# Optimization experiments

Hardware: AMD Instinct MI355X
Metric: run time of the kernel (lower is better)

## Reference

```python
import jax, jax.numpy as jnp
import numpy as np

NS, NW, E, DIN, OUT, H = 100_000, 400_000, 500_000, 64, 64, 4


def setup_inputs() -> dict:
    key = jax.random.key(0)
    ks = jax.random.split(key, 26)
    s = 1.0 / np.sqrt(DIN)
    sg = 1.0 / np.sqrt(OUT)
    inp = {
        "x_sites": jax.random.normal(ks[0], (NS, DIN), jnp.float32),
        "x_wells": jax.random.normal(ks[1], (NW, DIN), jnp.float32),
        "edge_sw_src": jax.random.randint(ks[2], (E,), 0, NS, jnp.int32),
        "edge_sw_dst": jax.random.randint(ks[3], (E,), 0, NW, jnp.int32),
        "edge_ws_src": jax.random.randint(ks[4], (E,), 0, NW, jnp.int32),
        "edge_ws_dst": jax.random.randint(ks[5], (E,), 0, NS, jnp.int32),
        # GAT ('pfas_sites','distance','gw_wells'), heads=4, concat=False
        "W_sw": jax.random.normal(ks[6], (DIN, H * OUT), jnp.float32) * s,
        "att_src_sw": jax.random.normal(ks[7], (H, OUT), jnp.float32) * sg,
        "att_dst_sw": jax.random.normal(ks[8], (H, OUT), jnp.float32) * sg,
        "b_sw": jnp.zeros((OUT,), jnp.float32),
        # SAGE ('gw_wells','distance','pfas_sites')
        "Wl_ws": jax.random.normal(ks[9], (DIN, OUT), jnp.float32) * s,
        "bl_ws": jnp.zeros((OUT,), jnp.float32),
        "Wr_ws": jax.random.normal(ks[10], (DIN, OUT), jnp.float32) * s,
        # GAT ('pfas_sites','self_loop','pfas_sites'), add_self_loops=True -> identity edges
        "W_ss": jax.random.normal(ks[11], (DIN, H * OUT), jnp.float32) * s,
        "att_src_ss": jax.random.normal(ks[12], (H, OUT), jnp.float32) * sg,
        "att_dst_ss": jax.random.normal(ks[13], (H, OUT), jnp.float32) * sg,
        "b_ss": jnp.zeros((OUT,), jnp.float32),
        # SAGE ('gw_wells','self_loop','gw_wells') with identity edges
        "Wl_ww": jax.random.normal(ks[14], (DIN, OUT), jnp.float32) * s,
        "bl_ww": jnp.zeros((OUT,), jnp.float32),
        "Wr_ww": jax.random.normal(ks[15], (DIN, OUT), jnp.float32) * s,
        # output heads
        "Wg": jax.random.normal(ks[16], (OUT, 1), jnp.float32) * sg,
        "bg": jnp.zeros((1,), jnp.float32),
        "Wsit": jax.random.normal(ks[17], (OUT, 1), jnp.float32) * sg,
        "bsit": jnp.zeros((1,), jnp.float32),
    }
    return inp


def _gat(x_src, x_dst, src, dst, W, a_src, a_dst, b, n_dst):
    """PyG GATConv, concat=False (mean over heads), negative_slope=0.2."""
    h, c = a_src.shape
    xs = (x_src @ W).reshape(-1, h, c)  # [Ns,H,C]
    xd = (x_dst @ W).reshape(-1, h, c)  # [Nd,H,C]
    al_s = jnp.einsum("nhc,hc->nh", xs, a_src)
    al_d = jnp.einsum("nhc,hc->nh", xd, a_dst)
    e = jax.nn.leaky_relu(al_s[src] + al_d[dst], 0.2)  # [E,H]
    m = jax.ops.segment_max(e, dst, num_segments=n_dst)
    ex = jnp.exp(e - m[dst])
    denom = jax.ops.segment_sum(ex, dst, num_segments=n_dst)
    alpha = ex / denom[dst]  # edge-softmax per dst node
    msg = xs[src] * alpha[:, :, None]  # [E,H,C] dominant intermediate
    out = jax.ops.segment_sum(msg, dst, num_segments=n_dst)
    return out.mean(axis=1) + b


def _sage(x_src, x_dst, src, dst, Wl, bl, Wr, n_dst):
    """PyG SAGEConv, mean aggregation, root_weight=True."""
    ssum = jax.ops.segment_sum(x_src[src], dst, num_segments=n_dst)
    cnt = jax.ops.segment_sum(jnp.ones((src.shape[0],), x_src.dtype), dst, num_segments=n_dst)
    mean = ssum / jnp.maximum(cnt, 1.0)[:, None]  # empty neighborhood -> 0 (PyG mean scatter)
    return mean @ Wl + bl + x_dst @ Wr


def reference(x_sites, x_wells, edge_sw_src, edge_sw_dst, edge_ws_src, edge_ws_dst,
              W_sw, att_src_sw, att_dst_sw, b_sw, Wl_ws, bl_ws, Wr_ws,
              W_ss, att_src_ss, att_dst_ss, b_ss, Wl_ww, bl_ww, Wr_ww,
              Wg, bg, Wsit, bsit):
    # relation 1: GAT sites -> wells
    gw = _gat(x_sites, x_wells, edge_sw_src, edge_sw_dst, W_sw, att_src_sw, att_dst_sw, b_sw, NW)
    # relation 4: SAGE self-loop on wells; identity edges -> mean == x itself
    gw = gw + (x_wells @ Wl_ww + bl_ww + x_wells @ Wr_ww)  # HeteroConv aggr='sum'
    # relation 2: SAGE wells -> sites
    si = _sage(x_wells, x_sites, edge_ws_src, edge_ws_dst, Wl_ws, bl_ws, Wr_ws, NS)
    # relation 3: GAT self-loop on sites (add_self_loops=True -> identity edge set);
    # softmax over a single self edge is 1, so output = mean over heads of lin(x) + bias
    si = si + (x_sites @ W_ss).reshape(NS, H, OUT).mean(axis=1) + b_ss
    # post: relu -> dropout (eval mode: identity) -> linear -> leaky_relu(0.01)
    gw = jax.nn.relu(gw)
    si = jax.nn.relu(si)
    o_gw = jax.nn.leaky_relu(gw @ Wg + bg, 0.01)   # [NW, 1]
    o_si = jax.nn.leaky_relu(si @ Wsit + bsit, 0.01)  # [NS, 1]
    return o_gw, o_si
```

## Files before the change

### kernel.cpp

```cpp
#include <hip/hip_runtime.h>

#define NS_ 100000
#define NW_ 400000
#define NE_ 500000
#define EPB 2048

#define SAGE_BLKS (NS_ / 16)
#define GAT_BLKS  (NW_ / 16)

typedef float f32x4_t __attribute__((ext_vector_type(4)));
typedef unsigned u32x4_t __attribute__((ext_vector_type(4)));

__device__ __forceinline__ float lrelu02(float x) { return x > 0.f ? x : 0.2f * x; }
__device__ __forceinline__ float bf2f(unsigned short u) {
    return __uint_as_float(((unsigned)u) << 16);
}
__device__ __forceinline__ unsigned short f2bf(float f) {
    unsigned u = __float_as_uint(f);
    u += 0x7FFFu + ((u >> 16) & 1u);
    return (unsigned short)(u >> 16);
}
__device__ __forceinline__ unsigned pk(float lo, float hi) {
    return (unsigned)f2bf(lo) | ((unsigned)f2bf(hi) << 16);
}
__device__ __forceinline__ void mfma_bf16(f32x4_t& acc, u32x4_t a, u32x4_t b) {
    asm volatile("v_mfma_f32_16x16x32_bf16 %0, %1, %2, %0" : "+v"(acc) : "v"(a), "v"(b));
}

__global__ void __launch_bounds__(256)
k_prep(const float* __restrict__ W_sw, const float* __restrict__ att_src,
       const float* __restrict__ att_dst,
       const float* __restrict__ Wl_ww, const float* __restrict__ Wr_ww,
       const float* __restrict__ Wl_ws, const float* __restrict__ Wr_ws,
       const float* __restrict__ W_ss,
       float* __restrict__ vd, float* __restrict__ vs,
       u32x4_t* __restrict__ fw, u32x4_t* __restrict__ fs,
       u32x4_t* __restrict__ fgw)
{
    const int tid = threadIdx.x;
    const int bid = blockIdx.x;
    if (bid == 0) {
        int d = tid >> 2, h = tid & 3;
        const float4* wp = (const float4*)(W_sw + d * 256 + h * 64);
        const float4* ad = (const float4*)(att_dst + h * 64);
        const float4* as = (const float4*)(att_src + h * 64);
        float accd = 0.f, accs = 0.f;
#pragma unroll
        for (int c = 0; c < 16; ++c) {
            float4 wv = wp[c]; float4 dv = ad[c]; float4 sv = as[c];
            accd += wv.x * dv.x + wv.y * dv.y + wv.z * dv.z + wv.w * dv.w;
            accs += wv.x * sv.x + wv.y * sv.y + wv.z * sv.z + wv.w * sv.w;
        }
        vd[d * 4 + h] = accd;
        vs[d * 4 + h] = accs;
    } else if (bid <= 2) {
        int idx = (bid - 1) * 256 + tid;
        int f = idx >> 6, lane = idx & 63;
        int kc = f >> 2, ct = f & 3, q = lane >> 4, n = lane & 15;
        int c = ct * 16 + n;
        u32x4_t d;
#pragma unroll
        for (int i = 0; i < 4; ++i) {
            int k = kc * 32 + q * 8 + 2 * i;
            d[i] = pk(Wl_ww[k * 64 + c] + Wr_ww[k * 64 + c],
                      Wl_ww[(k + 1) * 64 + c] + Wr_ww[(k + 1) * 64 + c]);
        }
        fw[idx] = d;
    } else if (bid <= 6) {
        int idx = (bid - 3) * 256 + tid;
        int f = idx >> 6, lane = idx & 63;
        int kc = f >> 2, ct = f & 3, q = lane >> 4, n = lane & 15;
        int c = ct * 16 + n;
        u32x4_t d;
#pragma unroll
        for (int i = 0; i < 4; ++i) {
            int k = kc * 32 + q * 8 + 2 * i;
            float lo, hi;
            if (k < 64) {
                lo = Wl_ws[k * 64 + c];
                hi = Wl_ws[(k + 1) * 64 + c];
            } else {
                int kk = k - 64;
                lo = Wr_ws[kk * 64 + c] + 0.25f * (W_ss[kk * 256 + c] + W_ss[kk * 256 + 64 + c] +
                                                   W_ss[kk * 256 + 128 + c] + W_ss[kk * 256 + 192 + c]);
                hi = Wr_ws[(kk + 1) * 64 + c] + 0.25f * (W_ss[(kk + 1) * 256 + c] + W_ss[(kk + 1) * 256 + 64 + c] +
                                                         W_ss[(kk + 1) * 256 + 128 + c] + W_ss[(kk + 1) * 256 + 192 + c]);
            }
            d[i] = pk(lo, hi);
        }
        fs[idx] = d;
    } else {
        int idx = (bid - 7) * 256 + tid;
        int f = idx >> 6, lane = idx & 63;
        int kc = f >> 2, ct = f & 3, q = lane >> 4, n = lane & 15;
        int c = ct * 16 + n;
        u32x4_t d;
#pragma unroll
        for (int i = 0; i < 4; ++i) {
            int kk = kc * 32 + q * 8 + 2 * i;
            int h = kk >> 6, k0 = kk & 63;
            d[i] = pk(W_sw[k0 * 256 + h * 64 + c], W_sw[(k0 + 1) * 256 + h * 64 + c]);
        }
        fgw[idx] = d;
    }
}

__global__ void __launch_bounds__(256)
k_sites_al(const float* __restrict__ x_sites, const float* __restrict__ vs,
           unsigned short* __restrict__ xbf, float* __restrict__ al_s)
{
    __shared__ float vsl[256];
    const int tid = threadIdx.x;
    vsl[tid] = vs[tid];
    __syncthreads();
    const int s = blockIdx.x * 64 + (tid >> 2);
    const int qq = tid & 3;
    if (s >= NS_) return;
    const float* xr = x_sites + (size_t)s * 64 + qq * 16;
    float4 a = *(const float4*)(xr);
    float4 b = *(const float4*)(xr + 4);
    float4 c = *(const float4*)(xr + 8);
    float4 d = *(const float4*)(xr + 12);
    float pa[4];
#pragma unroll
    for (int h = 0; h < 4; ++h) {
        const float* v = &vsl[(qq * 16) * 4 + h];
        pa[h] = a.x * v[0]  + a.y * v[4]  + a.z * v[8]  + a.w * v[12]
              + b.x * v[16] + b.y * v[20] + b.z * v[24] + b.w * v[28]
              + c.x * v[32] + c.y * v[36] + c.z * v[40] + c.w * v[44]
              + d.x * v[48] + d.y * v[52] + d.z * v[56] + d.w * v[60];
    }
#pragma unroll
    for (int h = 0; h < 4; ++h) {
        pa[h] += __shfl_xor(pa[h], 1, 64);
        pa[h] += __shfl_xor(pa[h], 2, 64);
    }
    if (qq == 0)
        *(float4*)(al_s + (size_t)s * 4) = make_float4(pa[0], pa[1], pa[2], pa[3]);
    u32x4_t lo = { pk(a.x, a.y), pk(a.z, a.w), pk(b.x, b.y), pk(b.z, b.w) };
    u32x4_t hi = { pk(c.x, c.y), pk(c.z, c.w), pk(d.x, d.y), pk(d.z, d.w) };
    unsigned short* xo = xbf + (size_t)s * 64 + qq * 16;
    *(u32x4_t*)(xo) = lo;
    *(u32x4_t*)(xo + 8) = hi;
}

__global__ void __launch_bounds__(256)
k_hist2(const int* __restrict__ d1, int* __restrict__ h1,
        const int* __restrict__ d2, int* __restrict__ h2)
{
    int e = blockIdx.x * 256 + threadIdx.x;
    if (e >= NE_) return;
    if (blockIdx.y == 0) atomicAdd(&h1[d1[e]], 1);
    else                 atomicAdd(&h2[d2[e]], 1);
}

__global__ void __launch_bounds__(256)
k_scan1_2(const int* __restrict__ h1, int n1, int* __restrict__ b1, int nb1,
          const int* __restrict__ h2, int n2, int* __restrict__ b2)
{
    __shared__ int red[256];
    const int tid = threadIdx.x;
    const int bx = blockIdx.x;
    const int* hist; int n; int* bsum; int blk;
    if (bx < nb1) { hist = h1; n = n1; bsum = b1; blk = bx; }
    else          { hist = h2; n = n2; bsum = b2; blk = bx - nb1; }
    int base = blk * EPB + tid * 8;
    int s = 0;
#pragma unroll
    for (int i = 0; i < 8; ++i) { int idx = base + i; if (idx < n) s += hist[idx]; }
    red[tid] = s;
    __syncthreads();
    for (int off = 128; off > 0; off >>= 1) {
        if (tid < off) red[tid] += red[tid + off];
        __syncthreads();
    }
    if (tid == 0) bsum[blk] = red[0];
}

__global__ void __launch_bounds__(256)
k_scan2_2(int* __restrict__ b1, int nb1, int* __restrict__ b2, int nb2)
{
    __shared__ int sh[256];
    const int tid = threadIdx.x;
    int* bsum = blockIdx.x == 0 ? b1 : b2;
    int nb = blockIdx.x == 0 ? nb1 : nb2;
    sh[tid] = (tid < nb) ? bsum[tid] : 0;
    __syncthreads();
    for (int off = 1; off < 256; off <<= 1) {
        int u = (tid >= off) ? sh[tid - off] : 0;
        __syncthreads();
        sh[tid] += u;
        __syncthreads();
    }
    if (tid < nb) bsum[tid] = (tid == 0) ? 0 : sh[tid - 1];
}

__global__ void __launch_bounds__(256)
k_scan3_2(const int* __restrict__ h1, int n1, const int* __restrict__ b1,
          int* __restrict__ rp1, int* __restrict__ cu1, int nb1,
          const int* __restrict__ h2, int n2, const int* __restrict__ b2,
          int* __restrict__ rp2, int* __restrict__ cu2)
{
    __shared__ int tsum[256];
    const int tid = threadIdx.x;
    const int bx = blockIdx.x;
    const int* hist; int n; const int* bsum; int* rowptr; int* cursor; int blk;
    if (bx < nb1) { hist = h1; n = n1; bsum = b1; rowptr = rp1; cursor = cu1; blk = bx; }
    else          { hist = h2; n = n2; bsum = b2; rowptr = rp2; cursor = cu2; blk = bx - nb1; }
    int base = blk * EPB + tid * 8;
    int v[8]; int s = 0;
#pragma unroll
    for (int i = 0; i < 8; ++i) {
        int idx = base + i;
        v[i] = (idx < n) ? hist[idx] : 0;
        s += v[i];
    }
    tsum[tid] = s;
    __syncthreads();
    for (int off = 1; off < 256; off <<= 1) {
        int u = (tid >= off) ? tsum[tid - off] : 0;
        __syncthreads();
        tsum[tid] += u;
        __syncthreads();
    }
    int texcl = tsum[tid] - s;
    int run = bsum[blk] + texcl;
#pragma unroll
    for (int i = 0; i < 8; ++i) {
        int idx = base + i;
        if (idx < n) { rowptr[idx] = run; cursor[idx] = run; run += v[i]; }
    }
    if (blk == 0 && tid == 0) rowptr[n] = NE_;
}

__global__ void __launch_bounds__(256)
k_scatter2(const int* __restrict__ s1, const int* __restrict__ d1,
           int* __restrict__ c1, int* __restrict__ o1,
           const int* __restrict__ s2, const int* __restrict__ d2,
           int* __restrict__ c2, int* __restrict__ o2)
{
    int e = blockIdx.x * 256 + threadIdx.x;
    if (e >= NE_) return;
    if (blockIdx.y == 0) { int p = atomicAdd(&c1[d1[e]], 1); o1[p] = s1[e]; }
    else                 { int p = atomicAdd(&c2[d2[e]], 1); o2[p] = s2[e]; }
}

__global__ void __launch_bounds__(256)
k_fin(const float* __restrict__ x_sites, const float* __restrict__ x_wells,
      const int* __restrict__ rp_ws, const int* __restrict__ csr_ws,
      const u32x4_t* __restrict__ fs, const float* __restrict__ bl_ws,
      const float* __restrict__ b_ss, const float* __restrict__ Wsit,
      const float* __restrict__ bsit,
      const float* __restrict__ vd, const int* __restrict__ rp_sw,
      const int* __restrict__ csr_sw, const float* __restrict__ al_s,
      const unsigned short* __restrict__ xbf, const float* __restrict__ b_sw,
      const float* __restrict__ bl_ww, const u32x4_t* __restrict__ fw,
      const u32x4_t* __restrict__ fgw, const float* __restrict__ Wg,
      const float* __restrict__ bg, float* __restrict__ out)
{
    __shared__ float smem[4192];
    const int tid = threadIdx.x;
    const int bid = blockIdx.x;

    if (bid % 5 == 0) {
        const int sb = bid / 5;
        unsigned* mnB = (unsigned*)smem;
        unsigned* xB  = (unsigned*)(smem + 576);
        float* dl     = smem + 1152;
        float* biasl  = smem + 2240;
        float* wsl    = smem + 2304;
        float* res    = smem + 2368;
        if (tid < 64) { biasl[tid] = bl_ws[tid] + b_ss[tid]; wsl[tid] = Wsit[tid]; }
        const int sl = tid >> 4, p = tid & 15;
        const int s = sb * 16 + sl;
        const int r0 = rp_ws[s], r1 = rp_ws[s + 1];
        float4 m4 = {0.f, 0.f, 0.f, 0.f};
        for (int j = r0; j < r1; ++j) {
            int wsrc = csr_ws[j];
            float4 xv = ((const float4*)(x_wells + (size_t)wsrc * 64))[p];
            m4.x += xv.x; m4.y += xv.y; m4.z += xv.z; m4.w += xv.w;
        }
        if (r1 > r0) {
            float rc = 1.f / (float)(r1 - r0);
            m4.x *= rc; m4.y *= rc; m4.z *= rc; m4.w *= rc;
        }
        {
            const int c0s = (2 * p + 8 * sl) & 31;
            mnB[sl * 36 + c0s]     = pk(m4.x, m4.y);
            mnB[sl * 36 + c0s + 1] = pk(m4.z, m4.w);
            float4 xv = *(const float4*)(x_sites + (size_t)s * 64 + 4 * p);
            xB[sl * 36 + c0s]     = pk(xv.x, xv.y);
            xB[sl * 36 + c0s + 1] = pk(xv.z, xv.w);
        }
        __syncthreads();
        const int wave = __builtin_amdgcn_readfirstlane(tid >> 6);
        const int lane = tid & 63, q = lane >> 4, n = lane & 15;
        const int b0 = (4 * q + 8 * n) & 31;
        const int b1 = (16 + 4 * q + 8 * n) & 31;
        u32x4_t am0 = *(const u32x4_t*)&mnB[n * 36 + b0];
        u32x4_t am1 = *(const u32x4_t*)&mnB[n * 36 + b1];
        u32x4_t ax0 = *(const u32x4_t*)&xB[n * 36 + b0];
        u32x4_t ax1 = *(const u32x4_t*)&xB[n * 36 + b1];
        f32x4_t acc = {0, 0, 0, 0};
        asm volatile("s_nop 3" : "+v"(am0), "+v"(am1), "+v"(ax0), "+v"(ax1), "+v"(acc));
        mfma_bf16(acc, am0, fs[wave * 64 + lane]);
        mfma_bf16(acc, am1, fs[(4 + wave) * 64 + lane]);
        mfma_bf16(acc, ax0, fs[(8 + wave) * 64 + lane]);
        mfma_bf16(acc, ax1, fs[(12 + wave) * 64 + lane]);
        asm volatile("s_nop 7\n\ts_nop 7" : "+v"(acc));
#pragma unroll
        for (int reg = 0; reg < 4; ++reg)
            dl[(q * 4 + reg) * 68 + wave * 16 + n] = acc[reg];
        __syncthreads();
        const int c0 = 4 * p;
        float4 dv = *(const float4*)&dl[sl * 68 + c0];
        float t0 = dv.x + biasl[c0];
        float t1 = dv.y + biasl[c0 + 1];
        float t2 = dv.z + biasl[c0 + 2];
        float t3 = dv.w + biasl[c0 + 3];
        float pr = fmaxf(t0, 0.f) * wsl[c0] + fmaxf(t1, 0.f) * wsl[c0 + 1] +
                   fmaxf(t2, 0.f) * wsl[c0 + 2] + fmaxf(t3, 0.f) * wsl[c0 + 3];
        pr += __shfl_xor(pr, 1, 64);
        pr += __shfl_xor(pr, 2, 64);
        pr += __shfl_xor(pr, 4, 64);
        pr += __shfl_xor(pr, 8, 64);
        if (p == 0) res[sl] = pr + bsit[0];
        __syncthreads();
        if (tid < 16) {
            float v = res[tid];
            out[(size_t)NW_ + sb * 16 + tid] = v > 0.f ? v : 0.01f * v;
        }
        return;
    }

    {
        const int gb = bid - 1 - bid / 5;
        float* vdl    = smem;
        unsigned* xwB = (unsigned*)(smem + 272);
        unsigned* agB = (unsigned*)(smem + 848);
        float* dl     = smem + 2960;
        float* biasl  = smem + 4048;
        float* wgl    = smem + 4112;
        float* res    = smem + 4176;
        vdl[(tid >> 4) * 17 + (tid & 15)] = vd[tid];
        if (tid < 64) { biasl[tid] = b_sw[tid] + bl_ww[tid]; wgl[tid] = Wg[tid]; }
        __syncthreads();
        const int wl = tid >> 4, p = tid & 15;
        const int w = gb * 16 + wl;
        const int r0 = rp_sw[w], r1 = rp_sw[w + 1];
        const int c0w = (2 * p + 8 * wl) & 31;
        float h0, h1, h2, h3;
        {
            float4 xv = *(const float4*)(x_wells + (size_t)w * 64 + 4 * p);
            xwB[wl * 36 + c0w]     = pk(xv.x, xv.y);
            xwB[wl * 36 + c0w + 1] = pk(xv.z, xv.w);
            const float* vp = &vdl[p * 17];
            h0 = xv.x * vp[0] + xv.y * vp[4] + xv.z * vp[8]  + xv.w * vp[12];
            h1 = xv.x * vp[1] + xv.y * vp[5] + xv.z * vp[9]  + xv.w * vp[13];
            h2 = xv.x * vp[2] + xv.y * vp[6] + xv.z * vp[10] + xv.w * vp[14];
            h3 = xv.x * vp[3] + xv.y * vp[7] + xv.z * vp[11] + xv.w * vp[15];
        }
#pragma unroll
        for (int off = 1; off < 16; off <<= 1) {
            h0 += __shfl_xor(h0, off, 64);
            h1 += __shfl_xor(h1, off, 64);
            h2 += __shfl_xor(h2, off, 64);
            h3 += __shfl_xor(h3, off, 64);
        }
        float den0 = 0, den1 = 0, den2 = 0, den3 = 0;
        float a00=0,a01=0,a02=0,a03=0, a10=0,a11=0,a12=0,a13=0;
        float a20=0,a21=0,a22=0,a23=0, a30=0,a31=0,a32=0,a33=0;
        for (int j = r0; j < r1; ++j) {
            int s = csr_sw[j];
            float4 as = ((const float4*)al_s)[s];
            ushort4 u = *(const ushort4*)(xbf + (size_t)s * 64 + 4 * p);
            float e0 = __expf(lrelu02(as.x + h0));
            float e1 = __expf(lrelu02(as.y + h1));
            float e2 = __expf(lrelu02(as.z + h2));
            float e3 = __expf(lrelu02(as.w + h3));
            den0 += e0; den1 += e1; den2 += e2; den3 += e3;
            float x0 = bf2f(u.x), x1 = bf2f(u.y), x2 = bf2f(u.z), x3 = bf2f(u.w);
            a00 += e0 * x0; a01 += e0 * x1; a02 += e0 * x2; a03 += e0 * x3;
            a10 += e1 * x0; a11 += e1 * x1; a12 += e1 * x2; a13 += e1 * x3;
            a20 += e2 * x0; a21 += e2 * x1; a22 += e2 * x2; a23 += e2 * x3;
            a30 += e3 * x0; a31 += e3 * x1; a32 += e3 * x2; a33 += e3 * x3;
        }
        if (r1 > r0) {
            float i0 = 0.25f / den0, i1 = 0.25f / den1, i2 = 0.25f / den2, i3 = 0.25f / den3;
            a00 *= i0; a01 *= i0; a02 *= i0; a03 *= i0;
            a10 *= i1; a11 *= i1; a12 *= i1; a13 *= i1;
            a20 *= i2; a21 *= i2; a22 *= i2; a23 *= i2;
            a30 *= i3; a31 *= i3; a32 *= i3; a33 *= i3;
        }
        agB[wl * 132 + 0 * 32 + c0w]     = pk(a00, a01);
        agB[wl * 132 + 0 * 32 + c0w + 1] = pk(a02, a03);
        agB[wl * 132 + 1 * 32 + c0w]     = pk(a10, a11);
        agB[wl * 132 + 1 * 32 + c0w + 1] = pk(a12, a13);
        agB[wl * 132 + 2 * 32 + c0w]     = pk(a20, a21);
        agB[wl * 132 + 2 * 32 + c0w + 1] = pk(a22, a23);
        agB[wl * 132 + 3 * 32 + c0w]     = pk(a30, a31);
        agB[wl * 132 + 3 * 32 + c0w + 1] = pk(a32, a33);
        __syncthreads();
        const int wave = __builtin_amdgcn_readfirstlane(tid >> 6);
        const int lane = tid & 63, q = lane >> 4, n = lane & 15;
        const int b0 = (4 * q + 8 * n) & 31;
        const int b1 = (16 + 4 * q + 8 * n) & 31;
        u32x4_t ax0 = *(const u32x4_t*)&xwB[n * 36 + b0];
        u32x4_t ax1 = *(const u32x4_t*)&xwB[n * 36 + b1];
        f32x4_t acc = {0, 0, 0, 0};
        asm volatile("s_nop 3" : "+v"(ax0), "+v"(ax1), "+v"(acc));
        mfma_bf16(acc, ax0, fw[wave * 64 + lane]);
        mfma_bf16(acc, ax1, fw[(4 + wave) * 64 + lane]);
#pragma unroll
        for (int kc = 0; kc < 8; ++kc) {
            const int hh = kc >> 1;
            const int sofs = (((kc & 1) * 16) + 4 * q + 8 * n) & 31;
            u32x4_t a = *(const u32x4_t*)&agB[n * 132 + hh * 32 + sofs];
            mfma_bf16(acc, a, fgw[(kc * 4 + wave) * 64 + lane]);
        }
        asm volatile("s_nop 7\n\ts_nop 7" : "+v"(acc));
#pragma unroll
        for (int reg = 0; reg < 4; ++reg)
            dl[(q * 4 + reg) * 68 + wave * 16 + n] = acc[reg];
        __syncthreads();
        const int c0 = 4 * p;
        float4 dv = *(const float4*)&dl[wl * 68 + c0];
        float t0 = dv.x + biasl[c0];
        float t1 = dv.y + biasl[c0 + 1];
        float t2 = dv.z + biasl[c0 + 2];
        float t3 = dv.w + biasl[c0 + 3];
        float pr = fmaxf(t0, 0.f) * wgl[c0] + fmaxf(t1, 0.f) * wgl[c0 + 1] +
                   fmaxf(t2, 0.f) * wgl[c0 + 2] + fmaxf(t3, 0.f) * wgl[c0 + 3];
        pr += __shfl_xor(pr, 1, 64);
        pr += __shfl_xor(pr, 2, 64);
        pr += __shfl_xor(pr, 4, 64);
        pr += __shfl_xor(pr, 8, 64);
        if (p == 0) res[wl] = pr + bg[0];
        __syncthreads();
        if (tid < 16) {
            float v = res[tid];
            out[gb * 16 + tid] = v > 0.f ? v : 0.01f * v;
        }
    }
}

extern "C" void kernel_launch(void* const* d_in, const int* in_sizes, int n_in,
                              void* d_out, int out_size, void* d_ws, size_t ws_size,
                              hipStream_t stream)
{
    const float* x_sites    = (const float*)d_in[0];
    const float* x_wells    = (const float*)d_in[1];
    const int*   e_sw_src   = (const int*)d_in[2];
    const int*   e_sw_dst   = (const int*)d_in[3];
    const int*   e_ws_src   = (const int*)d_in[4];
    const int*   e_ws_dst   = (const int*)d_in[5];
    const float* W_sw       = (const float*)d_in[6];
    const float* att_src_sw = (const float*)d_in[7];
    const float* att_dst_sw = (const float*)d_in[8];
    const float* b_sw       = (const float*)d_in[9];
    const float* Wl_ws      = (const float*)d_in[10];
    const float* bl_ws      = (const float*)d_in[11];
    const float* Wr_ws      = (const float*)d_in[12];
    const float* W_ss       = (const float*)d_in[13];
    const float* b_ss       = (const float*)d_in[16];
    const float* Wl_ww      = (const float*)d_in[17];
    const float* bl_ww      = (const float*)d_in[18];
    const float* Wr_ww      = (const float*)d_in[19];
    const float* Wg         = (const float*)d_in[20];
    const float* bg         = (const float*)d_in[21];
    const float* Wsit       = (const float*)d_in[22];
    const float* bsit       = (const float*)d_in[23];
    float* out = (float*)d_out;

    unsigned short* xbf = (unsigned short*)d_ws;
    float* al_s = (float*)(xbf + (size_t)NS_ * 64);
    float* vd   = al_s + (size_t)NS_ * 4;
    float* vs   = vd + 256;
    u32x4_t* fw = (u32x4_t*)(vs + 256);
    u32x4_t* fs = fw + 512;
    u32x4_t* fgw= fs + 1024;
    int* ip     = (int*)(fgw + 2048);
    int* h_sw   = ip;
    int* h_ws   = h_sw + NW_;
    int* rp_sw  = h_ws + NS_;
    int* cur_sw = rp_sw + NW_ + 4;
    int* csr_sw = cur_sw + NW_;
    int* bs_sw  = csr_sw + NE_;
    int* rp_ws  = bs_sw + 256;
    int* cur_ws = rp_ws + NS_ + 4;
    int* csr_ws = cur_ws + NS_;
    int* bs_ws  = csr_ws + NE_;

    hipMemsetAsync(h_sw, 0, (size_t)(NW_ + NS_) * sizeof(int), stream);

    const int egrid = (NE_ + 255) / 256;
    const int nb_sw = (NW_ + EPB - 1) / EPB;
    const int nb_ws = (NS_ + EPB - 1) / EPB;

    hipLaunchKernelGGL(k_prep, dim3(15), dim3(256), 0, stream,
                       W_sw, att_src_sw, att_dst_sw, Wl_ww, Wr_ww, Wl_ws, Wr_ws, W_ss,
                       vd, vs, fw, fs, fgw);

    hipLaunchKernelGGL(k_hist2, dim3(egrid, 2), dim3(256), 0, stream,
                       e_sw_dst, h_sw, e_ws_dst, h_ws);
    hipLaunchKernelGGL(k_scan1_2, dim3(nb_sw + nb_ws), dim3(256), 0, stream,
                       h_sw, NW_, bs_sw, nb_sw, h_ws, NS_, bs_ws);
    hipLaunchKernelGGL(k_scan2_2, dim3(2), dim3(256), 0, stream,
                       bs_sw, nb_sw, bs_ws, nb_ws);
    hipLaunchKernelGGL(k_scan3_2, dim3(nb_sw + nb_ws), dim3(256), 0, stream,
                       h_sw, NW_, bs_sw, rp_sw, cur_sw, nb_sw,
                       h_ws, NS_, bs_ws, rp_ws, cur_ws);
    hipLaunchKernelGGL(k_scatter2, dim3(egrid, 2), dim3(256), 0, stream,
                       e_sw_src, e_sw_dst, cur_sw, csr_sw,
                       e_ws_src, e_ws_dst, cur_ws, csr_ws);

    hipLaunchKernelGGL(k_sites_al, dim3((NS_ + 63) / 64), dim3(256), 0, stream,
                       x_sites, vs, xbf, al_s);

    hipLaunchKernelGGL(k_fin, dim3(SAGE_BLKS + GAT_BLKS), dim3(256), 0, stream,
                       x_sites, x_wells, rp_ws, csr_ws, fs, bl_ws, b_ss, Wsit, bsit,
                       vd, rp_sw, csr_sw, al_s, xbf, b_sw, bl_ww, fw, fgw,
                       Wg, bg, out);
}
```

Baseline: 452.3 us.

## Merge histogram with site projection, fold block-sum scan, prefetch edge indices

Fuses the edge-histogram kernel with the sites attention/bf16-conversion kernel into one launch. It also removes the separate block-sum scan kernel by having each scan3 block recompute the prefix of block sums in shared memory. The SAGE and GAT aggregation loops are unrolled by two, with the next source indices prefetched one step ahead to overlap the dependent loads. Paired LDS stores become single 64-bit stores. Together these cut launch count and gather latency, at the cost of a redundant small scan per block and a few extra clamped index loads.

Measured after the change: 447.5 us. Within noise of the previous version (-1.1%).

```diff
diff --git a/kernel.cpp b/kernel.cpp
--- a/kernel.cpp
+++ b/kernel.cpp
@@ -7,6 +7,8 @@
 
 #define SAGE_BLKS (NS_ / 16)
 #define GAT_BLKS  (NW_ / 16)
+#define EGRID ((NE_ + 255) / 256)
+#define SAL_BLKS ((NS_ + 63) / 64)
 
 typedef float f32x4_t __attribute__((ext_vector_type(4)));
 typedef unsigned u32x4_t __attribute__((ext_vector_type(4)));
@@ -106,14 +108,27 @@
 }
 
 __global__ void __launch_bounds__(256)
-k_sites_al(const float* __restrict__ x_sites, const float* __restrict__ vs,
-           unsigned short* __restrict__ xbf, float* __restrict__ al_s)
-{
+k_hist_sal(const float* __restrict__ x_sites, const float* __restrict__ vs,
+           unsigned short* __restrict__ xbf, float* __restrict__ al_s,
+           const int* __restrict__ d1, int* __restrict__ h1,
+           const int* __restrict__ d2, int* __restrict__ h2)
+{
+    const int tid = threadIdx.x;
+    const int bid = blockIdx.x;
+    if (bid >= SAL_BLKS) {
+        int hb = bid - SAL_BLKS;
+        int rel = hb / EGRID;
+        int e = (hb % EGRID) * 256 + tid;
+        if (e < NE_) {
+            if (rel == 0) atomicAdd(&h1[d1[e]], 1);
+            else          atomicAdd(&h2[d2[e]], 1);
+        }
+        return;
+    }
     __shared__ float vsl[256];
-    const int tid = threadIdx.x;
     vsl[tid] = vs[tid];
     __syncthreads();
-    const int s = blockIdx.x * 64 + (tid >> 2);
+    const int s = bid * 64 + (tid >> 2);
     const int qq = tid & 3;
     if (s >= NS_) return;
     const float* xr = x_sites + (size_t)s * 64 + qq * 16;
@@ -145,16 +160,6 @@
 }
 
 __global__ void __launch_bounds__(256)
-k_hist2(const int* __restrict__ d1, int* __restrict__ h1,
-        const int* __restrict__ d2, int* __restrict__ h2)
-{
-    int e = blockIdx.x * 256 + threadIdx.x;
-    if (e >= NE_) return;
-    if (blockIdx.y == 0) atomicAdd(&h1[d1[e]], 1);
-    else                 atomicAdd(&h2[d2[e]], 1);
-}
-
-__global__ void __launch_bounds__(256)
 k_scan1_2(const int* __restrict__ h1, int n1, int* __restrict__ b1, int nb1,
           const int* __restrict__ h2, int n2, int* __restrict__ b2)
 {
@@ -178,35 +183,27 @@
 }
 
 __global__ void __launch_bounds__(256)
-k_scan2_2(int* __restrict__ b1, int nb1, int* __restrict__ b2, int nb2)
-{
-    __shared__ int sh[256];
+k_scan3m(const int* __restrict__ h1, int n1, const int* __restrict__ b1,
+         int* __restrict__ rp1, int* __restrict__ cu1, int nb1,
+         const int* __restrict__ h2, int n2, const int* __restrict__ b2,
+         int* __restrict__ rp2, int* __restrict__ cu2, int nb2)
+{
+    __shared__ int tsum[256];
+    __shared__ int pre[256];
     const int tid = threadIdx.x;
-    int* bsum = blockIdx.x == 0 ? b1 : b2;
-    int nb = blockIdx.x == 0 ? nb1 : nb2;
-    sh[tid] = (tid < nb) ? bsum[tid] : 0;
+    const int bx = blockIdx.x;
+    const int* hist; int n; const int* bsum; int* rowptr; int* cursor; int blk; int nb;
+    if (bx < nb1) { hist = h1; n = n1; bsum = b1; rowptr = rp1; cursor = cu1; blk = bx; nb = nb1; }
+    else          { hist = h2; n = n2; bsum = b2; rowptr = rp2; cursor = cu2; blk = bx - nb1; nb = nb2; }
+    pre[tid] = (tid < nb) ? bsum[tid] : 0;
     __syncthreads();
     for (int off = 1; off < 256; off <<= 1) {
-        int u = (tid >= off) ? sh[tid - off] : 0;
-        __syncthreads();
-        sh[tid] += u;
-        __syncthreads();
-    }
-    if (tid < nb) bsum[tid] = (tid == 0) ? 0 : sh[tid - 1];
-}
-
-__global__ void __launch_bounds__(256)
-k_scan3_2(const int* __restrict__ h1, int n1, const int* __restrict__ b1,
-          int* __restrict__ rp1, int* __restrict__ cu1, int nb1,
-          const int* __restrict__ h2, int n2, const int* __restrict__ b2,
-          int* __restrict__ rp2, int* __restrict__ cu2)
-{
-    __shared__ int tsum[256];
-    const int tid = threadIdx.x;
-    const int bx = blockIdx.x;
-    const int* hist; int n; const int* bsum; int* rowptr; int* cursor; int blk;
-    if (bx < nb1) { hist = h1; n = n1; bsum = b1; rowptr = rp1; cursor = cu1; blk = bx; }
-    else          { hist = h2; n = n2; bsum = b2; rowptr = rp2; cursor = cu2; blk = bx - nb1; }
+        int u = (tid >= off) ? pre[tid - off] : 0;
+        __syncthreads();
+        pre[tid] += u;
+        __syncthreads();
+    }
+    const int blkoff = (blk == 0) ? 0 : pre[blk - 1];
     int base = blk * EPB + tid * 8;
     int v[8]; int s = 0;
 #pragma unroll
@@ -224,7 +221,7 @@
         __syncthreads();
     }
     int texcl = tsum[tid] - s;
-    int run = bsum[blk] + texcl;
+    int run = blkoff + texcl;
 #pragma unroll
     for (int i = 0; i < 8; ++i) {
         int idx = base + i;
@@ -274,11 +271,22 @@
         const int sl = tid >> 4, p = tid & 15;
         const int s = sb * 16 + sl;
         const int r0 = rp_ws[s], r1 = rp_ws[s + 1];
+        int sA = csr_ws[min(r0, NE_ - 1)];
+        int sB = csr_ws[min(r0 + 1, NE_ - 1)];
         float4 m4 = {0.f, 0.f, 0.f, 0.f};
-        for (int j = r0; j < r1; ++j) {
-            int wsrc = csr_ws[j];
-            float4 xv = ((const float4*)(x_wells + (size_t)wsrc * 64))[p];
-            m4.x += xv.x; m4.y += xv.y; m4.z += xv.z; m4.w += xv.w;
+        int j = r0;
+        for (; j + 2 <= r1; j += 2) {
+            float4 xv0 = ((const float4*)(x_wells + (size_t)sA * 64))[p];
+            float4 xv1 = ((const float4*)(x_wells + (size_t)sB * 64))[p];
+            int sN0 = csr_ws[min(j + 2, NE_ - 1)];
+            int sN1 = csr_ws[min(j + 3, NE_ - 1)];
+            m4.x += xv0.x; m4.y += xv0.y; m4.z += xv0.z; m4.w += xv0.w;
+            m4.x += xv1.x; m4.y += xv1.y; m4.z += xv1.z; m4.w += xv1.w;
+            sA = sN0; sB = sN1;
+        }
+        if (j < r1) {
+            float4 xv0 = ((const float4*)(x_wells + (size_t)sA * 64))[p];
+            m4.x += xv0.x; m4.y += xv0.y; m4.z += xv0.z; m4.w += xv0.w;
         }
         if (r1 > r0) {
             float rc = 1.f / (float)(r1 - r0);
@@ -286,11 +294,9 @@
         }
         {
             const int c0s = (2 * p + 8 * sl) & 31;
-            mnB[sl * 36 + c0s]     = pk(m4.x, m4.y);
-            mnB[sl * 36 + c0s + 1] = pk(m4.z, m4.w);
+            *(uint2*)&mnB[sl * 36 + c0s] = make_uint2(pk(m4.x, m4.y), pk(m4.z, m4.w));
             float4 xv = *(const float4*)(x_sites + (size_t)s * 64 + 4 * p);
-            xB[sl * 36 + c0s]     = pk(xv.x, xv.y);
-            xB[sl * 36 + c0s + 1] = pk(xv.z, xv.w);
+            *(uint2*)&xB[sl * 36 + c0s]  = make_uint2(pk(xv.x, xv.y), pk(xv.z, xv.w));
         }
         __syncthreads();
         const int wave = __builtin_amdgcn_readfirstlane(tid >> 6);
@@ -348,12 +354,13 @@
         const int wl = tid >> 4, p = tid & 15;
         const int w = gb * 16 + wl;
         const int r0 = rp_sw[w], r1 = rp_sw[w + 1];
+        int sA = csr_sw[min(r0, NE_ - 1)];
+        int sB = csr_sw[min(r0 + 1, NE_ - 1)];
         const int c0w = (2 * p + 8 * wl) & 31;
         float h0, h1, h2, h3;
         {
             float4 xv = *(const float4*)(x_wells + (size_t)w * 64 + 4 * p);
-            xwB[wl * 36 + c0w]     = pk(xv.x, xv.y);
-            xwB[wl * 36 + c0w + 1] = pk(xv.z, xv.w);
+            *(uint2*)&xwB[wl * 36 + c0w] = make_uint2(pk(xv.x, xv.y), pk(xv.z, xv.w));
             const float* vp = &vdl[p * 17];
             h0 = xv.x * vp[0] + xv.y * vp[4] + xv.z * vp[8]  + xv.w * vp[12];
             h1 = xv.x * vp[1] + xv.y * vp[5] + xv.z * vp[9]  + xv.w * vp[13];
@@ -370,10 +377,7 @@
         float den0 = 0, den1 = 0, den2 = 0, den3 = 0;
         float a00=0,a01=0,a02=0,a03=0, a10=0,a11=0,a12=0,a13=0;
         float a20=0,a21=0,a22=0,a23=0, a30=0,a31=0,a32=0,a33=0;
-        for (int j = r0; j < r1; ++j) {
-            int s = csr_sw[j];
-            float4 as = ((const float4*)al_s)[s];
-            ushort4 u = *(const ushort4*)(xbf + (size_t)s * 64 + 4 * p);
+        auto EDGE = [&](float4 as, ushort4 u) {
             float e0 = __expf(lrelu02(as.x + h0));
             float e1 = __expf(lrelu02(as.y + h1));
             float e2 = __expf(lrelu02(as.z + h2));
@@ -384,6 +388,23 @@
             a10 += e1 * x0; a11 += e1 * x1; a12 += e1 * x2; a13 += e1 * x3;
             a20 += e2 * x0; a21 += e2 * x1; a22 += e2 * x2; a23 += e2 * x3;
             a30 += e3 * x0; a31 += e3 * x1; a32 += e3 * x2; a33 += e3 * x3;
+        };
+        int j = r0;
+        for (; j + 2 <= r1; j += 2) {
+            float4 as0 = ((const float4*)al_s)[sA];
+            ushort4 u0 = *(const ushort4*)(xbf + (size_t)sA * 64 + 4 * p);
+            float4 as1 = ((const float4*)al_s)[sB];
+            ushort4 u1 = *(const ushort4*)(xbf + (size_t)sB * 64 + 4 * p);
+            int sN0 = csr_sw[min(j + 2, NE_ - 1)];
+            int sN1 = csr_sw[min(j + 3, NE_ - 1)];
+            EDGE(as0, u0);
+            EDGE(as1, u1);
+            sA = sN0; sB = sN1;
+        }
+        if (j < r1) {
+            float4 as0 = ((const float4*)al_s)[sA];
+            ushort4 u0 = *(const ushort4*)(xbf + (size_t)sA * 64 + 4 * p);
+            EDGE(as0, u0);
         }
         if (r1 > r0) {
             float i0 = 0.25f / den0, i1 = 0.25f / den1, i2 = 0.25f / den2, i3 = 0.25f / den3;
@@ -392,14 +413,10 @@
             a20 *= i2; a21 *= i2; a22 *= i2; a23 *= i2;
             a30 *= i3; a31 *= i3; a32 *= i3; a33 *= i3;
         }
-        agB[wl * 132 + 0 * 32 + c0w]     = pk(a00, a01);
-        agB[wl * 132 + 0 * 32 + c0w + 1] = pk(a02, a03);
-        agB[wl * 132 + 1 * 32 + c0w]     = pk(a10, a11);
-        agB[wl * 132 + 1 * 32 + c0w + 1] = pk(a12, a13);
-        agB[wl * 132 + 2 * 32 + c0w]     = pk(a20, a21);
-        agB[wl * 132 + 2 * 32 + c0w + 1] = pk(a22, a23);
-        agB[wl * 132 + 3 * 32 + c0w]     = pk(a30, a31);
-        agB[wl * 132 + 3 * 32 + c0w + 1] = pk(a32, a33);
+        *(uint2*)&agB[wl * 132 + 0 * 32 + c0w] = make_uint2(pk(a00, a01), pk(a02, a03));
+        *(uint2*)&agB[wl * 132 + 1 * 32 + c0w] = make_uint2(pk(a10, a11), pk(a12, a13));
+        *(uint2*)&agB[wl * 132 + 2 * 32 + c0w] = make_uint2(pk(a20, a21), pk(a22, a23));
+        *(uint2*)&agB[wl * 132 + 3 * 32 + c0w] = make_uint2(pk(a30, a31), pk(a32, a33));
         __syncthreads();
         const int wave = __builtin_amdgcn_readfirstlane(tid >> 6);
         const int lane = tid & 63, q = lane >> 4, n = lane & 15;
@@ -493,7 +510,6 @@
 
     hipMemsetAsync(h_sw, 0, (size_t)(NW_ + NS_) * sizeof(int), stream);
 
-    const int egrid = (NE_ + 255) / 256;
     const int nb_sw = (NW_ + EPB - 1) / EPB;
     const int nb_ws = (NS_ + EPB - 1) / EPB;
 
@@ -501,21 +517,17 @@
                        W_sw, att_src_sw, att_dst_sw, Wl_ww, Wr_ww, Wl_ws, Wr_ws, W_ss,
                        vd, vs, fw, fs, fgw);
 
-    hipLaunchKernelGGL(k_hist2, dim3(egrid, 2), dim3(256), 0, stream,
-                       e_sw_dst, h_sw, e_ws_dst, h_ws);
+    hipLaunchKernelGGL(k_hist_sal, dim3(SAL_BLKS + 2 * EGRID), dim3(256), 0, stream,
+                       x_sites, vs, xbf, al_s, e_sw_dst, h_sw, e_ws_dst, h_ws);
+
     hipLaunchKernelGGL(k_scan1_2, dim3(nb_sw + nb_ws), dim3(256), 0, stream,
                        h_sw, NW_, bs_sw, nb_sw, h_ws, NS_, bs_ws);
-    hipLaunchKernelGGL(k_scan2_2, dim3(2), dim3(256), 0, stream,
-                       bs_sw, nb_sw, bs_ws, nb_ws);
-    hipLaunchKernelGGL(k_scan3_2, dim3(nb_sw + nb_ws), dim3(256), 0, stream,
+    hipLaunchKernelGGL(k_scan3m, dim3(nb_sw + nb_ws), dim3(256), 0, stream,
                        h_sw, NW_, bs_sw, rp_sw, cur_sw, nb_sw,
-                       h_ws, NS_, bs_ws, rp_ws, cur_ws);
-    hipLaunchKernelGGL(k_scatter2, dim3(egrid, 2), dim3(256), 0, stream,
+                       h_ws, NS_, bs_ws, rp_ws, cur_ws, nb_ws);
+    hipLaunchKernelGGL(k_scatter2, dim3(EGRID, 2), dim3(256), 0, stream,
                        e_sw_src, e_sw_dst, cur_sw, csr_sw,
                        e_ws_src, e_ws_dst, cur_ws, csr_ws);
-
-    hipLaunchKernelGGL(k_sites_al, dim3((NS_ + 63) / 64), dim3(256), 0, stream,
-                       x_sites, vs, xbf, al_s);
 
     hipLaunchKernelGGL(k_fin, dim3(SAGE_BLKS + GAT_BLKS), dim3(256), 0, stream,
                        x_sites, x_wells, rp_ws, csr_ws, fs, bl_ws, b_ss, Wsit, bsit,
```
